# Kernel optimization log

Hardware: AMD Instinct MI355X
Metric: run time of the kernel (lower is better)

Reference implementation:

```python
import jax, jax.numpy as jnp
import numpy as np

EPS = 1e-8
B, T, D = 1, 768, 64
L = 4          # n_layers
PASSES = 2     # n_recursive_passes


def _project_to_simplex(x):
    p = jax.nn.softplus(x)
    p = p / (p.sum(axis=-1, keepdims=True) + EPS)
    return jnp.maximum(p, EPS)


def _qfi_attention_weights(x, temperature):
    # x: (B,T,D). Fisher-Rao distance on the simplex, full pairwise.
    p = _project_to_simplex(x)
    p = p / (p.sum(axis=-1, keepdims=True) + EPS)  # renorm inside fisher_rao
    # faithful to torch: sqrt(p_i*q_j + eps), requires (B,T,T,D) intermediate
    inner = jnp.sqrt(p[:, :, None, :] * p[:, None, :, :] + EPS).sum(axis=-1)
    inner = jnp.clip(inner, -1.0 + 1e-6, 1.0 - 1e-6)
    d = 2.0 * jnp.arccos(inner)                   # (B,T,T)
    logits = -d / jnp.maximum(temperature, 1e-6)
    return jax.nn.softmax(logits, axis=-1)


def setup_inputs() -> dict:
    key = jax.random.key(0)
    ks = jax.random.split(key, 12)
    s = 0.05
    return {
        "basin_seq": jax.random.normal(ks[0], (B, T, D), dtype=jnp.float32),
        "basin_coords": jax.random.normal(ks[1], (D,), dtype=jnp.float32) * 0.1,
        "temp_w": jax.random.normal(ks[2], (L, D), dtype=jnp.float32) * s,   # Linear(D,1) per layer
        "temp_b": jnp.zeros((L,), dtype=jnp.float32),
        "res_scale_layers": jnp.full((L,), 0.1, dtype=jnp.float32),
        "fb_w": jax.random.normal(ks[3], (L, D, 2 * D), dtype=jnp.float32) * s,
        "fb_b": jnp.zeros((L, D), dtype=jnp.float32),
        "comp_w1": jax.random.normal(ks[4], (D // 2, D), dtype=jnp.float32) * s,
        "comp_b1": jnp.zeros((D // 2,), dtype=jnp.float32),
        "comp_w2": jax.random.normal(ks[5], (D, D // 2), dtype=jnp.float32) * s,
        "comp_b2": jnp.zeros((D,), dtype=jnp.float32),
        "upd_w": jax.random.normal(ks[6], (D, 2 * D), dtype=jnp.float32) * s,
        "upd_b": jnp.zeros((D,), dtype=jnp.float32),
        "res_scale": jnp.float32(1.0),
    }


def reference(basin_seq, basin_coords, temp_w, temp_b, res_scale_layers,
              fb_w, fb_b, comp_w1, comp_b1, comp_w2, comp_b2,
              upd_w, upd_b, res_scale):
    x = basin_seq
    current_basin = basin_coords
    prev_states = [None] * L
    for p_idx in range(PASSES):
        new_states = []
        for l in range(L):
            prev = prev_states[l] if p_idx > 0 else None
            if prev is not None:
                g = jax.nn.sigmoid(jnp.concatenate([x, prev], axis=-1) @ fb_w[l].T + fb_b[l])
                x = x * g + prev * (1.0 - g)
            # basin-modulated temperature; torch uses .item() -> detached scalar
            tm = jax.nn.sigmoid(basin_coords_dot(current_basin, temp_w[l], temp_b[l])) + 0.5
            temperature = jax.lax.stop_gradient(tm)
            w = _qfi_attention_weights(x, temperature)        # (B,T,T), dropout=eval (identity)
            x_attn = jnp.einsum('bij,bjd->bid', w, x)
            x = x + res_scale_layers[l] * (x_attn - x)
            new_states.append(x)
        prev_states = new_states
        if p_idx < PASSES - 1:
            pooled = x.mean(axis=1)                           # (B,D)
            h = jnp.tanh(pooled @ comp_w1.T + comp_b1)
            h = jnp.tanh(h @ comp_w2.T + comp_b2)             # (B,D)
            agg = h.mean(axis=0)                              # (D,)
            gate = jax.nn.sigmoid(jnp.concatenate([current_basin, agg]) @ upd_w.T + upd_b)
            current_basin = current_basin * (1.0 - gate) + agg * gate
    return x + 0.01 * res_scale * (x - basin_seq)


def basin_coords_dot(basin, w, b):
    # Linear(D,1) applied to basin (D,) -> scalar; mean() of scalar is itself
    return jnp.dot(basin, w) + b
```

## Files before the change

kernel.cpp:

```cpp
#include <hip/hip_runtime.h>
#include <math.h>

#define T_ 768
#define TD (T_*64)
#define EPSF 1e-8f

typedef __attribute__((ext_vector_type(8))) short short8;
typedef __attribute__((ext_vector_type(4))) float f32x4;

__device__ __forceinline__ float wave_sum64(float v) {
#pragma unroll
  for (int m = 32; m >= 1; m >>= 1) v += __shfl_xor(v, m, 64);
  return v;
}
__device__ __forceinline__ float sigmoidf_(float x) { return 1.0f / (1.0f + expf(-x)); }

__device__ __forceinline__ unsigned short f2bf(float x) {
  unsigned int u = __float_as_uint(x);
  u += 0x7fffu + ((u >> 16) & 1u);
  return (unsigned short)(u >> 16);
}

__device__ __forceinline__ float acos_pos(float x) {
  float s = sqrtf(fmaxf(1.0f - x, 0.0f));
  return s * (1.5707288f + x * (-0.2121144f + x * (0.0742610f + x * (-0.0187293f))));
}

__device__ __forceinline__ void feat_bf(float v, int row, int lane,
                                        unsigned short* __restrict__ Fb) {
  float sp = fmaxf(v, 0.0f) + log1pf(expf(-fabsf(v)));
  float s = wave_sum64(sp);
  float p1 = fmaxf(sp / (s + EPSF), EPSF);
  float s2 = wave_sum64(p1);
  float p = p1 / (s2 + EPSF);
  Fb[row * 128 + lane] = f2bf(sqrtf(p));
  Fb[row * 128 + 64 + lane] = f2bf(sqrtf(5e-9f / p));
}

__global__ void __launch_bounds__(256)
phaseA_kernel(const float* __restrict__ bseq, const float* __restrict__ basin_coords,
              const float* __restrict__ temp_w, const float* __restrict__ temp_b,
              const float* __restrict__ fb_w,
              unsigned short* __restrict__ Fb, unsigned short* __restrict__ XTb,
              float* __restrict__ fbwT, float* __restrict__ temps) {
  int b = blockIdx.x, tid = threadIdx.x, w = tid >> 6, l = tid & 63;
  int row = b * 4 + w;
  float v = bseq[row * 64 + l];
  feat_bf(v, row, l, Fb);
  XTb[l * 768 + row] = f2bf(v);
  if (b < 128) {
    int idx = b * 256 + tid;
    int ll = idx >> 13, r = idx & 8191, d = r >> 7, k = r & 127;
    fbwT[ll * 8192 + k * 64 + d] = fb_w[ll * 8192 + d * 128 + k];
  }
  if (b == 191) {
    float t = basin_coords[l] * temp_w[w * 64 + l];
    t = wave_sum64(t);
    if (l == 0) temps[w] = sigmoidf_(t + temp_b[w]) + 0.5f;
  }
}

__global__ void __launch_bounds__(256)
qkpv_kernel(const unsigned short* __restrict__ Fbi,
            const unsigned short* __restrict__ XTi,
            const float* __restrict__ temps, int tidx,
            float* __restrict__ pvp_g, float* __restrict__ psum_g) {
  __shared__ __align__(16) unsigned short Pl[16][200];
  __shared__ float psumP[4][16];
  int tid = threadIdx.x, w = tid >> 6, l = tid & 63;
  int lr = l & 15, lk = l >> 4;
  int rt = blockIdx.x >> 2, c = blockIdx.x & 3;
  int i0 = rt * 16;

  const short8* arow = reinterpret_cast<const short8*>(Fbi + (i0 + lr) * 128);
  short8 afr[4];
#pragma unroll
  for (int ks = 0; ks < 4; ks++) afr[ks] = arow[ks * 4 + lk];
  float inv_t = 1.0f / fmaxf(temps[tidx], 1e-6f);

  float sp[4] = {0.f, 0.f, 0.f, 0.f};
#pragma unroll
  for (int jj = 0; jj < 3; jj++) {
    int jt = w + jj * 4;
    int jg = c * 12 + jt;
    const short8* brow = reinterpret_cast<const short8*>(Fbi + (jg * 16 + lr) * 128);
    f32x4 acc = {0.f, 0.f, 0.f, 0.f};
#pragma unroll
    for (int ks = 0; ks < 4; ks++)
      acc = __builtin_amdgcn_mfma_f32_16x16x32_bf16(afr[ks], brow[ks * 4 + lk], acc, 0, 0, 0);
#pragma unroll
    for (int r = 0; r < 4; r++) {
      float inner = fminf(fmaxf(acc[r], 0.0f), 1.0f - 1e-6f);
      float e = expf(-2.0f * acos_pos(inner) * inv_t);
      Pl[lk * 4 + r][jt * 16 + lr] = f2bf(e);
      sp[r] += e;
    }
  }
#pragma unroll
  for (int m = 1; m <= 8; m <<= 1)
#pragma unroll
    for (int r = 0; r < 4; r++) sp[r] += __shfl_xor(sp[r], m, 64);
  if (lr == 0)
#pragma unroll
    for (int r = 0; r < 4; r++) psumP[w][lk * 4 + r] = sp[r];
  __syncthreads();

  f32x4 pacc = {0.f, 0.f, 0.f, 0.f};
  const short8* xtrow =
      reinterpret_cast<const short8*>(XTi + (w * 16 + lr) * 768 + c * 192);
#pragma unroll
  for (int ks = 0; ks < 6; ks++) {
    short8 pa = *reinterpret_cast<const short8*>(&Pl[lr][ks * 32 + lk * 8]);
    pacc = __builtin_amdgcn_mfma_f32_16x16x32_bf16(pa, xtrow[ks * 4 + lk], pacc, 0, 0, 0);
  }
  float* dst = pvp_g + (blockIdx.x << 10);
#pragma unroll
  for (int r = 0; r < 4; r++) dst[(lk * 4 + r) * 64 + w * 16 + lr] = pacc[r];
  if (tid < 16)
    psum_g[blockIdx.x * 16 + tid] =
        psumP[0][tid] + psumP[1][tid] + psumP[2][tid] + psumP[3][tid];
}

__global__ void __launch_bounds__(256)
combine_kernel(const float* __restrict__ pvp_g, const float* __restrict__ psum_g,
               const float* __restrict__ xin, int lidx,
               const float* __restrict__ rs_layers, int mode,
               float* __restrict__ xout,
               unsigned short* __restrict__ Fbo, unsigned short* __restrict__ XTo,
               const float* __restrict__ WT, const float* __restrict__ bb,
               const float* __restrict__ prevX,
               float* __restrict__ gateOut, float* __restrict__ poolPart,
               const float* __restrict__ bseq, const float* __restrict__ res_scale,
               float* __restrict__ outp) {
  __shared__ float xs[4][64], ps[4][64];
  int tid = threadIdx.x, w = tid >> 6, l = tid & 63;
  int bid = blockIdx.x;
  int rt = bid >> 2, row16 = (bid & 3) * 4 + w;
  int grow = bid * 4 + w;

  float pv = 0.f, s = 0.f;
#pragma unroll
  for (int c = 0; c < 4; c++) {
    pv += pvp_g[((rt * 4 + c) << 10) + row16 * 64 + l];
    s += psum_g[(rt * 4 + c) * 16 + row16];
  }
  float attn = pv / s;
  float xi = xin[grow * 64 + l];
  float rs = rs_layers[lidx];
  float xo = xi + rs * (attn - xi);
  xs[w][l] = xo;
  if (mode == 1 || mode == 2) ps[w][l] = prevX[grow * 64 + l];
  __syncthreads();

  if (mode == 3) {
    outp[grow * 64 + l] = xo + 0.01f * res_scale[0] * (xo - bseq[grow * 64 + l]);
    return;
  }
  if (mode == 0) {
    xout[grow * 64 + l] = xo;
    XTo[l * 768 + grow] = f2bf(xo);
    feat_bf(xo, grow, l, Fbo);
    return;
  }
  float a = bb[l];
#pragma unroll 8
  for (int k = 0; k < 64; k++) a += xs[w][k] * WT[k * 64 + l];
#pragma unroll 8
  for (int k = 0; k < 64; k++) a += ps[w][k] * WT[(64 + k) * 64 + l];
  float g = sigmoidf_(a);
  float xn = xo * g + ps[w][l] * (1.0f - g);
  if (mode == 1) {
    xout[grow * 64 + l] = xo;
    gateOut[grow * 64 + l] = xn;
    XTo[l * 768 + grow] = f2bf(xn);
    feat_bf(xn, grow, l, Fbo);
    if (w == 0)
      poolPart[bid * 64 + l] = xs[0][l] + xs[1][l] + xs[2][l] + xs[3][l];
  } else {
    xout[grow * 64 + l] = xn;
    XTo[l * 768 + grow] = f2bf(xn);
    feat_bf(xn, grow, l, Fbo);
  }
}

__global__ void __launch_bounds__(256)
mlp_kernel(const float* __restrict__ poolPart, const float* __restrict__ basin_coords,
           const float* __restrict__ temp_w, const float* __restrict__ temp_b,
           const float* __restrict__ w1, const float* __restrict__ b1,
           const float* __restrict__ w2, const float* __restrict__ b2,
           const float* __restrict__ uw, const float* __restrict__ ub,
           float* __restrict__ temps) {
  __shared__ float part4[4][64];
  __shared__ float pooled[64], h1s[32], aggs[64], bnew[64];
  int tid = threadIdx.x, w = tid >> 6, l = tid & 63;
  {
    float s = 0.f;
    for (int bb = w * 48; bb < w * 48 + 48; bb++) s += poolPart[bb * 64 + l];
    part4[w][l] = s;
  }
  __syncthreads();
  if (tid < 64)
    pooled[tid] = (part4[0][tid] + part4[1][tid] + part4[2][tid] + part4[3][tid]) *
                  (1.0f / 768.0f);
  __syncthreads();
  if (tid < 32) {
    float h = b1[tid];
    for (int k = 0; k < 64; k++) h += w1[tid * 64 + k] * pooled[k];
    h1s[tid] = tanhf(h);
  }
  __syncthreads();
  if (tid < 64) {
    float h = b2[tid];
    for (int k = 0; k < 32; k++) h += w2[tid * 32 + k] * h1s[k];
    aggs[tid] = tanhf(h);
  }
  __syncthreads();
  if (tid < 64) {
    float g = ub[tid];
    for (int k = 0; k < 64; k++) g += uw[tid * 128 + k] * basin_coords[k];
    for (int k = 0; k < 64; k++) g += uw[tid * 128 + 64 + k] * aggs[k];
    g = sigmoidf_(g);
    bnew[tid] = basin_coords[tid] * (1.0f - g) + aggs[tid] * g;
  }
  __syncthreads();
  {
    float t = bnew[l] * temp_w[w * 64 + l];
    t = wave_sum64(t);
    if (l == 0) temps[4 + w] = sigmoidf_(t + temp_b[w]) + 0.5f;
  }
}

extern "C" void kernel_launch(void* const* d_in, const int* in_sizes, int n_in,
                              void* d_out, int out_size, void* d_ws, size_t ws_size,
                              hipStream_t stream) {
  const float* bseq         = (const float*)d_in[0];
  const float* basin_coords = (const float*)d_in[1];
  const float* temp_w       = (const float*)d_in[2];
  const float* temp_b       = (const float*)d_in[3];
  const float* rs_layers    = (const float*)d_in[4];
  const float* fb_w         = (const float*)d_in[5];
  const float* fb_b         = (const float*)d_in[6];
  const float* comp_w1      = (const float*)d_in[7];
  const float* comp_b1      = (const float*)d_in[8];
  const float* comp_w2      = (const float*)d_in[9];
  const float* comp_b2      = (const float*)d_in[10];
  const float* upd_w        = (const float*)d_in[11];
  const float* upd_b        = (const float*)d_in[12];
  const float* res_scale    = (const float*)d_in[13];
  float* out = (float*)d_out;

  float* ws = (float*)d_ws;
  float* xA       = ws;
  float* xB       = xA + TD;
  float* prevb    = xB + TD;
  float* fbwT     = prevb + 4 * TD;
  float* poolPart = fbwT + 32768;
  float* psum_g   = poolPart + 12288;
  float* pvp_g    = psum_g + 3072;
  float* temps    = pvp_g + 196608;
  unsigned short* Fb0 = (unsigned short*)(temps + 16);
  unsigned short* Fb1 = Fb0 + 98304;
  unsigned short* XT0 = Fb1 + 98304;
  unsigned short* XT1 = XT0 + 49152;

  phaseA_kernel<<<192, 256, 0, stream>>>(bseq, basin_coords, temp_w, temp_b, fb_w,
                                         Fb0, XT0, fbwT, temps);
  qkpv_kernel<<<192, 256, 0, stream>>>(Fb0, XT0, temps, 0, pvp_g, psum_g);
  combine_kernel<<<192, 256, 0, stream>>>(pvp_g, psum_g, bseq, 0, rs_layers, 0,
                                          prevb, Fb1, XT1, nullptr, nullptr, nullptr,
                                          nullptr, nullptr, nullptr, nullptr, nullptr);
  qkpv_kernel<<<192, 256, 0, stream>>>(Fb1, XT1, temps, 1, pvp_g, psum_g);
  combine_kernel<<<192, 256, 0, stream>>>(pvp_g, psum_g, prevb, 1, rs_layers, 0,
                                          prevb + TD, Fb0, XT0, nullptr, nullptr, nullptr,
                                          nullptr, nullptr, nullptr, nullptr, nullptr);
  qkpv_kernel<<<192, 256, 0, stream>>>(Fb0, XT0, temps, 2, pvp_g, psum_g);
  combine_kernel<<<192, 256, 0, stream>>>(pvp_g, psum_g, prevb + TD, 2, rs_layers, 0,
                                          prevb + 2 * TD, Fb1, XT1, nullptr, nullptr, nullptr,
                                          nullptr, nullptr, nullptr, nullptr, nullptr);
  qkpv_kernel<<<192, 256, 0, stream>>>(Fb1, XT1, temps, 3, pvp_g, psum_g);
  combine_kernel<<<192, 256, 0, stream>>>(pvp_g, psum_g, prevb + 2 * TD, 3, rs_layers, 1,
                                          prevb + 3 * TD, Fb0, XT0,
                                          fbwT, fb_b, prevb,
                                          xA, poolPart, nullptr, nullptr, nullptr);
  mlp_kernel<<<1, 256, 0, stream>>>(poolPart, basin_coords, temp_w, temp_b,
                                    comp_w1, comp_b1, comp_w2, comp_b2,
                                    upd_w, upd_b, temps);
  qkpv_kernel<<<192, 256, 0, stream>>>(Fb0, XT0, temps, 4, pvp_g, psum_g);
  combine_kernel<<<192, 256, 0, stream>>>(pvp_g, psum_g, xA, 0, rs_layers, 2,
                                          xB, Fb1, XT1,
                                          fbwT + 8192, fb_b + 64, prevb + TD,
                                          nullptr, nullptr, nullptr, nullptr, nullptr);
  qkpv_kernel<<<192, 256, 0, stream>>>(Fb1, XT1, temps, 5, pvp_g, psum_g);
  combine_kernel<<<192, 256, 0, stream>>>(pvp_g, psum_g, xB, 1, rs_layers, 2,
                                          xA, Fb0, XT0,
                                          fbwT + 16384, fb_b + 128, prevb + 2 * TD,
                                          nullptr, nullptr, nullptr, nullptr, nullptr);
  qkpv_kernel<<<192, 256, 0, stream>>>(Fb0, XT0, temps, 6, pvp_g, psum_g);
  combine_kernel<<<192, 256, 0, stream>>>(pvp_g, psum_g, xA, 2, rs_layers, 2,
                                          xB, Fb1, XT1,
                                          fbwT + 24576, fb_b + 192, prevb + 3 * TD,
                                          nullptr, nullptr, nullptr, nullptr, nullptr);
  qkpv_kernel<<<192, 256, 0, stream>>>(Fb1, XT1, temps, 7, pvp_g, psum_g);
  combine_kernel<<<192, 256, 0, stream>>>(pvp_g, psum_g, xB, 3, rs_layers, 3,
                                          nullptr, nullptr, nullptr, nullptr, nullptr, nullptr,
                                          nullptr, nullptr, bseq, res_scale, out);
}
```

Before: 99.14 us.

## Fuse attention and combine into one per-layer kernel, inline MLP into layer launch

Merges the qkpv and combine kernels so each block owns 4 full query rows and computes all 768 keys, removing the partial pv/psum global round trip and halving launches. The single-block MLP is recomputed redundantly in every block of the first second-pass layer, and temperatures are computed in-kernel, which removes another launch. In exchange, each wave computes 16-row MFMA tiles of which only 4 rows are useful (lk==0), wasting roughly 3/4 of the QK MFMA and exp work, and the 192 blocks each do more serial work.

```diff
diff --git a/kernel.cpp b/kernel.cpp
--- a/kernel.cpp
+++ b/kernel.cpp
@@ -38,11 +38,9 @@
 }
 
 __global__ void __launch_bounds__(256)
-phaseA_kernel(const float* __restrict__ bseq, const float* __restrict__ basin_coords,
-              const float* __restrict__ temp_w, const float* __restrict__ temp_b,
-              const float* __restrict__ fb_w,
+phaseA_kernel(const float* __restrict__ bseq, const float* __restrict__ fb_w,
               unsigned short* __restrict__ Fb, unsigned short* __restrict__ XTb,
-              float* __restrict__ fbwT, float* __restrict__ temps) {
+              float* __restrict__ fbwT) {
   int b = blockIdx.x, tid = threadIdx.x, w = tid >> 6, l = tid & 63;
   int row = b * 4 + w;
   float v = bseq[row * 64 + l];
@@ -53,46 +51,100 @@
     int ll = idx >> 13, r = idx & 8191, d = r >> 7, k = r & 127;
     fbwT[ll * 8192 + k * 64 + d] = fb_w[ll * 8192 + d * 128 + k];
   }
-  if (b == 191) {
-    float t = basin_coords[l] * temp_w[w * 64 + l];
-    t = wave_sum64(t);
-    if (l == 0) temps[w] = sigmoidf_(t + temp_b[w]) + 0.5f;
-  }
 }
 
 __global__ void __launch_bounds__(256)
-qkpv_kernel(const unsigned short* __restrict__ Fbi,
-            const unsigned short* __restrict__ XTi,
-            const float* __restrict__ temps, int tidx,
-            float* __restrict__ pvp_g, float* __restrict__ psum_g) {
-  __shared__ __align__(16) unsigned short Pl[16][200];
-  __shared__ float psumP[4][16];
+layer_k(const unsigned short* __restrict__ Fbi,
+        const unsigned short* __restrict__ XTi,
+        int lidx, int mode, int doMlp,
+        const float* __restrict__ tbase,
+        const float* __restrict__ temp_w, const float* __restrict__ temp_b,
+        const float* __restrict__ rs_layers,
+        const float* __restrict__ xin, float* __restrict__ xout,
+        unsigned short* __restrict__ Fbo, unsigned short* __restrict__ XTo,
+        const float* __restrict__ WT, const float* __restrict__ bbias,
+        const float* __restrict__ prevX,
+        float* __restrict__ gateOut, float* __restrict__ poolPart,
+        const float* __restrict__ mlp_pool, const float* __restrict__ basin_coords,
+        const float* __restrict__ w1, const float* __restrict__ b1,
+        const float* __restrict__ w2, const float* __restrict__ b2,
+        const float* __restrict__ uw, const float* __restrict__ ub,
+        float* __restrict__ bnew_g,
+        const float* __restrict__ bseq, const float* __restrict__ res_scale,
+        float* __restrict__ outp) {
+  __shared__ __align__(16) unsigned short Pl[4][776];
+  __shared__ float sums[4][4];
+  __shared__ float pvs[4][64];
+  __shared__ float xs[4][64], ps[4][64];
+  __shared__ float part4[4][64];
+  __shared__ float pooled[64], h1s[32], aggs[64], bnewS[64];
   int tid = threadIdx.x, w = tid >> 6, l = tid & 63;
   int lr = l & 15, lk = l >> 4;
-  int rt = blockIdx.x >> 2, c = blockIdx.x & 3;
-  int i0 = rt * 16;
-
-  const short8* arow = reinterpret_cast<const short8*>(Fbi + (i0 + lr) * 128);
+  int b = blockIdx.x, i0 = b * 4;
+
+  float temp;
+  if (doMlp) {
+    {
+      float s = 0.f;
+      for (int bb2 = w * 48; bb2 < w * 48 + 48; bb2++) s += mlp_pool[bb2 * 64 + l];
+      part4[w][l] = s;
+    }
+    __syncthreads();
+    if (tid < 64)
+      pooled[tid] = (part4[0][tid] + part4[1][tid] + part4[2][tid] + part4[3][tid]) *
+                    (1.0f / 768.0f);
+    __syncthreads();
+    if (tid < 32) {
+      float h = b1[tid];
+      for (int k = 0; k < 64; k++) h += w1[tid * 64 + k] * pooled[k];
+      h1s[tid] = tanhf(h);
+    }
+    __syncthreads();
+    if (tid < 64) {
+      float h = b2[tid];
+      for (int k = 0; k < 32; k++) h += w2[tid * 32 + k] * h1s[k];
+      aggs[tid] = tanhf(h);
+    }
+    __syncthreads();
+    if (tid < 64) {
+      float g = ub[tid];
+      for (int k = 0; k < 64; k++) g += uw[tid * 128 + k] * basin_coords[k];
+      for (int k = 0; k < 64; k++) g += uw[tid * 128 + 64 + k] * aggs[k];
+      g = sigmoidf_(g);
+      bnewS[tid] = basin_coords[tid] * (1.0f - g) + aggs[tid] * g;
+    }
+    __syncthreads();
+    if (b == 0 && tid < 64) bnew_g[tid] = bnewS[tid];
+    float v = bnewS[l] * temp_w[lidx * 64 + l];
+    v = wave_sum64(v);
+    temp = sigmoidf_(v + temp_b[lidx]) + 0.5f;
+  } else {
+    float v = tbase[l] * temp_w[lidx * 64 + l];
+    v = wave_sum64(v);
+    temp = sigmoidf_(v + temp_b[lidx]) + 0.5f;
+  }
+  float inv_t = 1.0f / fmaxf(temp, 1e-6f);
+
+  const short8* arow = reinterpret_cast<const short8*>(Fbi + (i0 + (lr & 3)) * 128);
   short8 afr[4];
 #pragma unroll
   for (int ks = 0; ks < 4; ks++) afr[ks] = arow[ks * 4 + lk];
-  float inv_t = 1.0f / fmaxf(temps[tidx], 1e-6f);
 
   float sp[4] = {0.f, 0.f, 0.f, 0.f};
-#pragma unroll
-  for (int jj = 0; jj < 3; jj++) {
-    int jt = w + jj * 4;
-    int jg = c * 12 + jt;
-    const short8* brow = reinterpret_cast<const short8*>(Fbi + (jg * 16 + lr) * 128);
-    f32x4 acc = {0.f, 0.f, 0.f, 0.f};
-#pragma unroll
-    for (int ks = 0; ks < 4; ks++)
-      acc = __builtin_amdgcn_mfma_f32_16x16x32_bf16(afr[ks], brow[ks * 4 + lk], acc, 0, 0, 0);
+#pragma unroll 4
+  for (int jj = 0; jj < 12; jj++) {
+    int jt = w * 12 + jj;
+    const short8* brow = reinterpret_cast<const short8*>(Fbi + (jt * 16 + lr) * 128);
+    f32x4 accA = {0.f, 0.f, 0.f, 0.f}, accB = {0.f, 0.f, 0.f, 0.f};
+    accA = __builtin_amdgcn_mfma_f32_16x16x32_bf16(afr[0], brow[0 * 4 + lk], accA, 0, 0, 0);
+    accB = __builtin_amdgcn_mfma_f32_16x16x32_bf16(afr[2], brow[2 * 4 + lk], accB, 0, 0, 0);
+    accA = __builtin_amdgcn_mfma_f32_16x16x32_bf16(afr[1], brow[1 * 4 + lk], accA, 0, 0, 0);
+    accB = __builtin_amdgcn_mfma_f32_16x16x32_bf16(afr[3], brow[3 * 4 + lk], accB, 0, 0, 0);
 #pragma unroll
     for (int r = 0; r < 4; r++) {
-      float inner = fminf(fmaxf(acc[r], 0.0f), 1.0f - 1e-6f);
+      float inner = fminf(fmaxf(accA[r] + accB[r], 0.0f), 1.0f - 1e-6f);
       float e = expf(-2.0f * acos_pos(inner) * inv_t);
-      Pl[lk * 4 + r][jt * 16 + lr] = f2bf(e);
+      if (lk == 0) Pl[r][jt * 16 + lr] = f2bf(e);
       sp[r] += e;
     }
   }
@@ -100,69 +152,47 @@
   for (int m = 1; m <= 8; m <<= 1)
 #pragma unroll
     for (int r = 0; r < 4; r++) sp[r] += __shfl_xor(sp[r], m, 64);
-  if (lr == 0)
-#pragma unroll
-    for (int r = 0; r < 4; r++) psumP[w][lk * 4 + r] = sp[r];
+  if (l == 0)
+#pragma unroll
+    for (int r = 0; r < 4; r++) sums[w][r] = sp[r];
   __syncthreads();
 
-  f32x4 pacc = {0.f, 0.f, 0.f, 0.f};
-  const short8* xtrow =
-      reinterpret_cast<const short8*>(XTi + (w * 16 + lr) * 768 + c * 192);
-#pragma unroll
-  for (int ks = 0; ks < 6; ks++) {
-    short8 pa = *reinterpret_cast<const short8*>(&Pl[lr][ks * 32 + lk * 8]);
-    pacc = __builtin_amdgcn_mfma_f32_16x16x32_bf16(pa, xtrow[ks * 4 + lk], pacc, 0, 0, 0);
-  }
-  float* dst = pvp_g + (blockIdx.x << 10);
-#pragma unroll
-  for (int r = 0; r < 4; r++) dst[(lk * 4 + r) * 64 + w * 16 + lr] = pacc[r];
-  if (tid < 16)
-    psum_g[blockIdx.x * 16 + tid] =
-        psumP[0][tid] + psumP[1][tid] + psumP[2][tid] + psumP[3][tid];
-}
-
-__global__ void __launch_bounds__(256)
-combine_kernel(const float* __restrict__ pvp_g, const float* __restrict__ psum_g,
-               const float* __restrict__ xin, int lidx,
-               const float* __restrict__ rs_layers, int mode,
-               float* __restrict__ xout,
-               unsigned short* __restrict__ Fbo, unsigned short* __restrict__ XTo,
-               const float* __restrict__ WT, const float* __restrict__ bb,
-               const float* __restrict__ prevX,
-               float* __restrict__ gateOut, float* __restrict__ poolPart,
-               const float* __restrict__ bseq, const float* __restrict__ res_scale,
-               float* __restrict__ outp) {
-  __shared__ float xs[4][64], ps[4][64];
-  int tid = threadIdx.x, w = tid >> 6, l = tid & 63;
-  int bid = blockIdx.x;
-  int rt = bid >> 2, row16 = (bid & 3) * 4 + w;
-  int grow = bid * 4 + w;
-
-  float pv = 0.f, s = 0.f;
-#pragma unroll
-  for (int c = 0; c < 4; c++) {
-    pv += pvp_g[((rt * 4 + c) << 10) + row16 * 64 + l];
-    s += psum_g[(rt * 4 + c) * 16 + row16];
-  }
-  float attn = pv / s;
-  float xi = xin[grow * 64 + l];
-  float rs = rs_layers[lidx];
-  float xo = xi + rs * (attn - xi);
+  {
+    f32x4 pA = {0.f, 0.f, 0.f, 0.f}, pB = {0.f, 0.f, 0.f, 0.f};
+    const short8* xtrow = reinterpret_cast<const short8*>(XTi + (w * 16 + lr) * 768);
+#pragma unroll 4
+    for (int ks = 0; ks < 12; ks++) {
+      short8 paA = *reinterpret_cast<const short8*>(&Pl[lr & 3][ks * 32 + lk * 8]);
+      short8 paB = *reinterpret_cast<const short8*>(&Pl[lr & 3][(ks + 12) * 32 + lk * 8]);
+      pA = __builtin_amdgcn_mfma_f32_16x16x32_bf16(paA, xtrow[ks * 4 + lk], pA, 0, 0, 0);
+      pB = __builtin_amdgcn_mfma_f32_16x16x32_bf16(paB, xtrow[(ks + 12) * 4 + lk], pB, 0, 0, 0);
+    }
+    if (lk == 0)
+#pragma unroll
+      for (int r = 0; r < 4; r++) pvs[r][w * 16 + lr] = pA[r] + pB[r];
+  }
+  __syncthreads();
+
+  int row = i0 + w;
+  float stot = sums[0][w] + sums[1][w] + sums[2][w] + sums[3][w];
+  float attn = pvs[w][l] / stot;
+  float xi = xin[row * 64 + l];
+  float xo = xi + rs_layers[lidx] * (attn - xi);
   xs[w][l] = xo;
-  if (mode == 1 || mode == 2) ps[w][l] = prevX[grow * 64 + l];
+  if (mode == 1 || mode == 2) ps[w][l] = prevX[row * 64 + l];
   __syncthreads();
 
   if (mode == 3) {
-    outp[grow * 64 + l] = xo + 0.01f * res_scale[0] * (xo - bseq[grow * 64 + l]);
+    outp[row * 64 + l] = xo + 0.01f * res_scale[0] * (xo - bseq[row * 64 + l]);
     return;
   }
   if (mode == 0) {
-    xout[grow * 64 + l] = xo;
-    XTo[l * 768 + grow] = f2bf(xo);
-    feat_bf(xo, grow, l, Fbo);
+    xout[row * 64 + l] = xo;
+    XTo[l * 768 + row] = f2bf(xo);
+    feat_bf(xo, row, l, Fbo);
     return;
   }
-  float a = bb[l];
+  float a = bbias[l];
 #pragma unroll 8
   for (int k = 0; k < 64; k++) a += xs[w][k] * WT[k * 64 + l];
 #pragma unroll 8
@@ -170,64 +200,15 @@
   float g = sigmoidf_(a);
   float xn = xo * g + ps[w][l] * (1.0f - g);
   if (mode == 1) {
-    xout[grow * 64 + l] = xo;
-    gateOut[grow * 64 + l] = xn;
-    XTo[l * 768 + grow] = f2bf(xn);
-    feat_bf(xn, grow, l, Fbo);
-    if (w == 0)
-      poolPart[bid * 64 + l] = xs[0][l] + xs[1][l] + xs[2][l] + xs[3][l];
+    xout[row * 64 + l] = xo;
+    gateOut[row * 64 + l] = xn;
   } else {
-    xout[grow * 64 + l] = xn;
-    XTo[l * 768 + grow] = f2bf(xn);
-    feat_bf(xn, grow, l, Fbo);
-  }
-}
-
-__global__ void __launch_bounds__(256)
-mlp_kernel(const float* __restrict__ poolPart, const float* __restrict__ basin_coords,
-           const float* __restrict__ temp_w, const float* __restrict__ temp_b,
-           const float* __restrict__ w1, const float* __restrict__ b1,
-           const float* __restrict__ w2, const float* __restrict__ b2,
-           const float* __restrict__ uw, const float* __restrict__ ub,
-           float* __restrict__ temps) {
-  __shared__ float part4[4][64];
-  __shared__ float pooled[64], h1s[32], aggs[64], bnew[64];
-  int tid = threadIdx.x, w = tid >> 6, l = tid & 63;
-  {
-    float s = 0.f;
-    for (int bb = w * 48; bb < w * 48 + 48; bb++) s += poolPart[bb * 64 + l];
-    part4[w][l] = s;
-  }
-  __syncthreads();
-  if (tid < 64)
-    pooled[tid] = (part4[0][tid] + part4[1][tid] + part4[2][tid] + part4[3][tid]) *
-                  (1.0f / 768.0f);
-  __syncthreads();
-  if (tid < 32) {
-    float h = b1[tid];
-    for (int k = 0; k < 64; k++) h += w1[tid * 64 + k] * pooled[k];
-    h1s[tid] = tanhf(h);
-  }
-  __syncthreads();
-  if (tid < 64) {
-    float h = b2[tid];
-    for (int k = 0; k < 32; k++) h += w2[tid * 32 + k] * h1s[k];
-    aggs[tid] = tanhf(h);
-  }
-  __syncthreads();
-  if (tid < 64) {
-    float g = ub[tid];
-    for (int k = 0; k < 64; k++) g += uw[tid * 128 + k] * basin_coords[k];
-    for (int k = 0; k < 64; k++) g += uw[tid * 128 + 64 + k] * aggs[k];
-    g = sigmoidf_(g);
-    bnew[tid] = basin_coords[tid] * (1.0f - g) + aggs[tid] * g;
-  }
-  __syncthreads();
-  {
-    float t = bnew[l] * temp_w[w * 64 + l];
-    t = wave_sum64(t);
-    if (l == 0) temps[4 + w] = sigmoidf_(t + temp_b[w]) + 0.5f;
-  }
+    xout[row * 64 + l] = xn;
+  }
+  XTo[l * 768 + row] = f2bf(xn);
+  feat_bf(xn, row, l, Fbo);
+  if (mode == 1 && w == 0)
+    poolPart[b * 64 + l] = xs[0][l] + xs[1][l] + xs[2][l] + xs[3][l];
 }
 
 extern "C" void kernel_launch(void* const* d_in, const int* in_sizes, int n_in,
@@ -255,53 +236,100 @@
   float* prevb    = xB + TD;
   float* fbwT     = prevb + 4 * TD;
   float* poolPart = fbwT + 32768;
-  float* psum_g   = poolPart + 12288;
-  float* pvp_g    = psum_g + 3072;
-  float* temps    = pvp_g + 196608;
-  unsigned short* Fb0 = (unsigned short*)(temps + 16);
+  float* bnew_g   = poolPart + 12288;
+  unsigned short* Fb0 = (unsigned short*)(bnew_g + 80);
   unsigned short* Fb1 = Fb0 + 98304;
   unsigned short* XT0 = Fb1 + 98304;
   unsigned short* XT1 = XT0 + 49152;
 
-  phaseA_kernel<<<192, 256, 0, stream>>>(bseq, basin_coords, temp_w, temp_b, fb_w,
-                                         Fb0, XT0, fbwT, temps);
-  qkpv_kernel<<<192, 256, 0, stream>>>(Fb0, XT0, temps, 0, pvp_g, psum_g);
-  combine_kernel<<<192, 256, 0, stream>>>(pvp_g, psum_g, bseq, 0, rs_layers, 0,
-                                          prevb, Fb1, XT1, nullptr, nullptr, nullptr,
-                                          nullptr, nullptr, nullptr, nullptr, nullptr);
-  qkpv_kernel<<<192, 256, 0, stream>>>(Fb1, XT1, temps, 1, pvp_g, psum_g);
-  combine_kernel<<<192, 256, 0, stream>>>(pvp_g, psum_g, prevb, 1, rs_layers, 0,
-                                          prevb + TD, Fb0, XT0, nullptr, nullptr, nullptr,
-                                          nullptr, nullptr, nullptr, nullptr, nullptr);
-  qkpv_kernel<<<192, 256, 0, stream>>>(Fb0, XT0, temps, 2, pvp_g, psum_g);
-  combine_kernel<<<192, 256, 0, stream>>>(pvp_g, psum_g, prevb + TD, 2, rs_layers, 0,
-                                          prevb + 2 * TD, Fb1, XT1, nullptr, nullptr, nullptr,
-                                          nullptr, nullptr, nullptr, nullptr, nullptr);
-  qkpv_kernel<<<192, 256, 0, stream>>>(Fb1, XT1, temps, 3, pvp_g, psum_g);
-  combine_kernel<<<192, 256, 0, stream>>>(pvp_g, psum_g, prevb + 2 * TD, 3, rs_layers, 1,
-                                          prevb + 3 * TD, Fb0, XT0,
-                                          fbwT, fb_b, prevb,
-                                          xA, poolPart, nullptr, nullptr, nullptr);
-  mlp_kernel<<<1, 256, 0, stream>>>(poolPart, basin_coords, temp_w, temp_b,
-                                    comp_w1, comp_b1, comp_w2, comp_b2,
-                                    upd_w, upd_b, temps);
-  qkpv_kernel<<<192, 256, 0, stream>>>(Fb0, XT0, temps, 4, pvp_g, psum_g);
-  combine_kernel<<<192, 256, 0, stream>>>(pvp_g, psum_g, xA, 0, rs_layers, 2,
-                                          xB, Fb1, XT1,
-                                          fbwT + 8192, fb_b + 64, prevb + TD,
-                                          nullptr, nullptr, nullptr, nullptr, nullptr);
-  qkpv_kernel<<<192, 256, 0, stream>>>(Fb1, XT1, temps, 5, pvp_g, psum_g);
-  combine_kernel<<<192, 256, 0, stream>>>(pvp_g, psum_g, xB, 1, rs_layers, 2,
-                                          xA, Fb0, XT0,
-                                          fbwT + 16384, fb_b + 128, prevb + 2 * TD,
-                                          nullptr, nullptr, nullptr, nullptr, nullptr);
-  qkpv_kernel<<<192, 256, 0, stream>>>(Fb0, XT0, temps, 6, pvp_g, psum_g);
-  combine_kernel<<<192, 256, 0, stream>>>(pvp_g, psum_g, xA, 2, rs_layers, 2,
-                                          xB, Fb1, XT1,
-                                          fbwT + 24576, fb_b + 192, prevb + 3 * TD,
-                                          nullptr, nullptr, nullptr, nullptr, nullptr);
-  qkpv_kernel<<<192, 256, 0, stream>>>(Fb1, XT1, temps, 7, pvp_g, psum_g);
-  combine_kernel<<<192, 256, 0, stream>>>(pvp_g, psum_g, xB, 3, rs_layers, 3,
-                                          nullptr, nullptr, nullptr, nullptr, nullptr, nullptr,
-                                          nullptr, nullptr, bseq, res_scale, out);
-}
+  phaseA_kernel<<<192, 256, 0, stream>>>(bseq, fb_w, Fb0, XT0, fbwT);
+
+  layer_k<<<192, 256, 0, stream>>>(
+       Fb0,  XT0,  0,  0,  0,
+       basin_coords,  temp_w,  temp_b,
+       rs_layers,  bseq,  prevb,
+       Fb1,  XT1,
+       nullptr,  nullptr,  nullptr,
+       nullptr,  nullptr,
+       nullptr,  nullptr,
+       nullptr,  nullptr,  nullptr,  nullptr,
+       nullptr,  nullptr,  nullptr,
+       nullptr,  nullptr,  nullptr);
+  layer_k<<<192, 256, 0, stream>>>(
+       Fb1,  XT1,  1,  0,  0,
+       basin_coords,  temp_w,  temp_b,
+       rs_layers,  prevb,  prevb + TD,
+       Fb0,  XT0,
+       nullptr,  nullptr,  nullptr,
+       nullptr,  nullptr,
+       nullptr,  nullptr,
+       nullptr,  nullptr,  nullptr,  nullptr,
+       nullptr,  nullptr,  nullptr,
+       nullptr,  nullptr,  nullptr);
+  layer_k<<<192, 256, 0, stream>>>(
+       Fb0,  XT0,  2,  0,  0,
+       basin_coords,  temp_w,  temp_b,
+       rs_layers,  prevb + TD,  prevb + 2 * TD,
+       Fb1,  XT1,
+       nullptr,  nullptr,  nullptr,
+       nullptr,  nullptr,
+       nullptr,  nullptr,
+       nullptr,  nullptr,  nullptr,  nullptr,
+       nullptr,  nullptr,  nullptr,
+       nullptr,  nullptr,  nullptr);
+  layer_k<<<192, 256, 0, stream>>>(
+       Fb1,  XT1,  3,  1,  0,
+       basin_coords,  temp_w,  temp_b,
+       rs_layers,  prevb + 2 * TD,  prevb + 3 * TD,
+       Fb0,  XT0,
+       fbwT,  fb_b,  prevb,
+       xA,  poolPart,
+       nullptr,  nullptr,
+       nullptr,  nullptr,  nullptr,  nullptr,
+       nullptr,  nullptr,  nullptr,
+       nullptr,  nullptr,  nullptr);
+  layer_k<<<192, 256, 0, stream>>>(
+       Fb0,  XT0,  0,  2,  1,
+       nullptr,  temp_w,  temp_b,
+       rs_layers,  xA,  xB,
+       Fb1,  XT1,
+       fbwT + 8192,  fb_b + 64,  prevb + TD,
+       nullptr,  nullptr,
+       poolPart,  basin_coords,
+       comp_w1,  comp_b1,  comp_w2,  comp_b2,
+       upd_w,  upd_b,  bnew_g,
+       nullptr,  nullptr,  nullptr);
+  layer_k<<<192, 256, 0, stream>>>(
+       Fb1,  XT1,  1,  2,  0,
+       bnew_g,  temp_w,  temp_b,
+       rs_layers,  xB,  xA,
+       Fb0,  XT0,
+       fbwT + 16384,  fb_b + 128,  prevb + 2 * TD,
+       nullptr,  nullptr,
+       nullptr,  nullptr,
+       nullptr,  nullptr,  nullptr,  nullptr,
+       nullptr,  nullptr,  nullptr,
+       nullptr,  nullptr,  nullptr);
+  layer_k<<<192, 256, 0, stream>>>(
+       Fb0,  XT0,  2,  2,  0,
+       bnew_g,  temp_w,  temp_b,
+       rs_layers,  xA,  xB,
+       Fb1,  XT1,
+       fbwT + 24576,  fb_b + 192,  prevb + 3 * TD,
+       nullptr,  nullptr,
+       nullptr,  nullptr,
+       nullptr,  nullptr,  nullptr,  nullptr,
+       nullptr,  nullptr,  nullptr,
+       nullptr,  nullptr,  nullptr);
+  layer_k<<<192, 256, 0, stream>>>(
+       Fb1,  XT1,  3,  3,  0,
+       bnew_g,  temp_w,  temp_b,
+       rs_layers,  xB,  nullptr,
+       nullptr,  nullptr,
+       nullptr,  nullptr,  nullptr,
+       nullptr,  nullptr,
+       nullptr,  nullptr,
+       nullptr,  nullptr,  nullptr,  nullptr,
+       nullptr,  nullptr,  nullptr,
+       bseq,  res_scale,  out);
+}
```

New measurement: 195.1 us. 1.97x slower.
